# Kernel tuning notes

Measured on AMD Instinct MI355X. Metric: run time of the kernel, lower is better.

Reference implementation:

```python
import jax, jax.numpy as jnp
import numpy as np

N_NODES = 100000
N_EDGES = 640000
HIDDEN = 128


def setup_inputs() -> dict:
    key = jax.random.key(0)
    k1, k2, k3, k4 = jax.random.split(key, 4)
    node_emb = jax.random.normal(k1, (N_NODES, HIDDEN), dtype=jnp.float32)
    edge_index = jax.random.randint(k2, (2, N_EDGES), 0, N_NODES, dtype=jnp.int64)
    # edge head params: Linear(2H -> H), Linear(H -> 2)
    s1 = 1.0 / np.sqrt(2 * HIDDEN)
    s2 = 1.0 / np.sqrt(HIDDEN)
    W1 = jax.random.uniform(k3, (2 * HIDDEN, HIDDEN), jnp.float32, -s1, s1)
    b1 = jnp.zeros((HIDDEN,), jnp.float32)
    W2 = jax.random.uniform(k4, (HIDDEN, 2), jnp.float32, -s2, s2)
    b2 = jnp.zeros((2,), jnp.float32)
    return {"node_emb": node_emb, "edge_index": edge_index,
            "W1": W1, "b1": b1, "W2": W2, "b2": b2}


def reference(node_emb, edge_index, W1, b1, W2, b2):
    # gather src/dst node embeddings by edge_index (irregular gather)
    src, dst = edge_index[0], edge_index[1]
    edge_emb = jnp.concatenate([node_emb[src], node_emb[dst]], axis=-1)  # [E, 2H]
    # edge head: Linear -> ReLU -> (Dropout = identity in eval) -> Linear
    h = jax.nn.relu(edge_emb @ W1 + b1)  # [E, H]
    flow_pred = h @ W2 + b2              # [E, 2]
    return flow_pred
```

## Files before the change

kernel.cpp:

```cpp
#include <hip/hip_runtime.h>

typedef __attribute__((ext_vector_type(8))) short short8;
typedef __attribute__((ext_vector_type(4))) float floatx4;

static __device__ __forceinline__ unsigned short f2bf(float f) {
    union { float f; unsigned int u; } v; v.f = f;
    unsigned int u = v.u;
    return (unsigned short)((u + 0x7FFFu + ((u >> 16) & 1u)) >> 16);
}

__global__ void cvt_nodes_kernel(const float* __restrict__ x,
                                 unsigned short* __restrict__ y, int n4) {
    int i = blockIdx.x * blockDim.x + threadIdx.x;
    if (i >= n4) return;
    const float4 v = ((const float4*)x)[i];
    ushort4 o;
    o.x = f2bf(v.x); o.y = f2bf(v.y); o.z = f2bf(v.z); o.w = f2bf(v.w);
    ((ushort4*)y)[i] = o;
}

__global__ void cvt_w1t_kernel(const float* __restrict__ w1,
                               unsigned short* __restrict__ w1t) {
    int t = blockIdx.x * blockDim.x + threadIdx.x;
    int k = t >> 7;
    int n = t & 127;
    w1t[n * 256 + k] = f2bf(w1[t]);
}

#define LDSW 136

__global__ __launch_bounds__(256, 2) void edge_mlp_kernel(
    const unsigned short* __restrict__ nodes,
    const unsigned short* __restrict__ w1t,
    const int* __restrict__ eidx,
    const float* __restrict__ b1,
    const float* __restrict__ w2,
    const float* __restrict__ b2,
    float* __restrict__ out,
    int E, int n_nodes)
{
    __shared__ unsigned short sB[128 * LDSW];

    const int tid = threadIdx.x;
    const int lane = tid & 63;
    const int wave = tid >> 6;
    const int l15 = lane & 15;
    const int lq  = lane >> 4;
    const long e0 = (long)blockIdx.x * 256 + (long)wave * 64;

    int offs[4], offd[4];
#pragma unroll
    for (int rt = 0; rt < 4; rt++) {
        long e = e0 + rt * 16 + l15;
        if (e >= E) e = E - 1;
        int s = eidx[e];
        int d = eidx[(long)E + e];
        s = (s < 0) ? 0 : (s >= n_nodes ? n_nodes - 1 : s);
        d = (d < 0) ? 0 : (d >= n_nodes ? n_nodes - 1 : d);
        offs[rt] = s << 8;
        offd[rt] = d << 8;
    }
    const char* nbase = (const char*)nodes;
    const int lko = lq * 16;

    floatx4 acc[4][8];
#pragma unroll
    for (int rt = 0; rt < 4; rt++)
#pragma unroll
        for (int t = 0; t < 8; t++) acc[rt][t] = (floatx4){0.f, 0.f, 0.f, 0.f};

    short8 a_cur[4], a_nxt[4];
#pragma unroll
    for (int rt = 0; rt < 4; rt++)
        a_cur[rt] = *(const short8*)(nbase + offs[rt] + lko);

    for (int ch = 0; ch < 2; ch++) {
        if (ch) __syncthreads();
        for (int c = tid; c < 2048; c += 256) {
            int n = c >> 4, kk = (c & 15) << 3;
            *(short8*)(&sB[n * LDSW + kk]) =
                *(const short8*)(&w1t[n * 256 + ch * 128 + kk]);
        }
        __syncthreads();

#pragma unroll
        for (int k2 = 0; k2 < 4; k2++) {
            const int ks = ch * 4 + k2;
            if (ks < 7) {
                const int ksn = ks + 1;
                const int cb = ((ksn & 3) * 64) + lko;
#pragma unroll
                for (int rt = 0; rt < 4; rt++)
                    a_nxt[rt] = *(const short8*)(
                        nbase + ((ksn < 4) ? offs[rt] : offd[rt]) + cb);
            }
            const int bko = k2 * 32 + lq * 8;
#pragma unroll
            for (int t = 0; t < 8; t++) {
                short8 b = *(const short8*)(&sB[(t * 16 + l15) * LDSW + bko]);
#pragma unroll
                for (int rt = 0; rt < 4; rt++)
                    acc[rt][t] = __builtin_amdgcn_mfma_f32_16x16x32_bf16(
                        a_cur[rt], b, acc[rt][t], 0, 0, 0);
            }
#pragma unroll
            for (int rt = 0; rt < 4; rt++) a_cur[rt] = a_nxt[rt];
        }
    }

    float b1v[8], w20[8], w21[8];
#pragma unroll
    for (int t = 0; t < 8; t++) {
        int c = t * 16 + l15;
        b1v[t] = b1[c];
        w20[t] = w2[c * 2];
        w21[t] = w2[c * 2 + 1];
    }
    const float bias0 = b2[0], bias1 = b2[1];
#pragma unroll
    for (int rt = 0; rt < 4; rt++) {
#pragma unroll
        for (int i = 0; i < 4; i++) {
            float p0 = 0.f, p1 = 0.f;
#pragma unroll
            for (int t = 0; t < 8; t++) {
                float h = acc[rt][t][i] + b1v[t];
                h = fmaxf(h, 0.f);
                p0 = fmaf(h, w20[t], p0);
                p1 = fmaf(h, w21[t], p1);
            }
#pragma unroll
            for (int m = 1; m < 16; m <<= 1) {
                p0 += __shfl_xor(p0, m, 64);
                p1 += __shfl_xor(p1, m, 64);
            }
            if (l15 == 0) {
                long e = e0 + rt * 16 + lq * 4 + i;
                if (e < E) {
                    float2 o;
                    o.x = p0 + bias0;
                    o.y = p1 + bias1;
                    *(float2*)(&out[e * 2]) = o;
                }
            }
        }
    }
}

extern "C" void kernel_launch(void* const* d_in, const int* in_sizes, int n_in,
                              void* d_out, int out_size, void* d_ws, size_t ws_size,
                              hipStream_t stream) {
    const float* node_emb = (const float*)d_in[0];
    const int*   eidx     = (const int*)d_in[1];
    const float* W1       = (const float*)d_in[2];
    const float* b1       = (const float*)d_in[3];
    const float* W2       = (const float*)d_in[4];
    const float* b2       = (const float*)d_in[5];
    float* out = (float*)d_out;

    const int n_node_elems = in_sizes[0];
    const int n_nodes = n_node_elems / 128;
    const int E = in_sizes[1] / 2;

    unsigned short* nodes_bf16 = (unsigned short*)d_ws;
    unsigned short* w1t =
        (unsigned short*)((char*)d_ws + (size_t)n_node_elems * 2);

    const int n4 = n_node_elems / 4;
    cvt_nodes_kernel<<<(n4 + 255) / 256, 256, 0, stream>>>(node_emb, nodes_bf16, n4);
    cvt_w1t_kernel<<<128, 256, 0, stream>>>(W1, w1t);

    const int nblk = (E + 255) / 256;
    edge_mlp_kernel<<<nblk, 256, 0, stream>>>(nodes_bf16, w1t, eidx,
                                              b1, W2, b2, out, E, n_nodes);
}
```

Measured before the change: 188.8 us.

## Split output columns across wave pairs, swizzle LDS, merge conversion kernels

```diff
diff --git a/kernel.cpp b/kernel.cpp
--- a/kernel.cpp
+++ b/kernel.cpp
@@ -9,27 +9,38 @@
     return (unsigned short)((u + 0x7FFFu + ((u >> 16) & 1u)) >> 16);
 }
 
-__global__ void cvt_nodes_kernel(const float* __restrict__ x,
-                                 unsigned short* __restrict__ y, int n4) {
-    int i = blockIdx.x * blockDim.x + threadIdx.x;
-    if (i >= n4) return;
-    const float4 v = ((const float4*)x)[i];
-    ushort4 o;
-    o.x = f2bf(v.x); o.y = f2bf(v.y); o.z = f2bf(v.z); o.w = f2bf(v.w);
-    ((ushort4*)y)[i] = o;
+__global__ void cvt_kernel(const float* __restrict__ x, unsigned short* __restrict__ y,
+                           int n4, const float* __restrict__ w1,
+                           unsigned short* __restrict__ w1t, int nblk_nodes) {
+    __shared__ unsigned short sT[32 * 130];
+    if ((int)blockIdx.x < nblk_nodes) {
+        int i = blockIdx.x * 256 + threadIdx.x;
+        if (i >= n4) return;
+        const float4 v = ((const float4*)x)[i];
+        ushort4 o;
+        o.x = f2bf(v.x); o.y = f2bf(v.y); o.z = f2bf(v.z); o.w = f2bf(v.w);
+        ((ushort4*)y)[i] = o;
+    } else {
+        const int b = blockIdx.x - nblk_nodes;
+        const int k0 = b * 32;
+        const int tid = threadIdx.x;
+#pragma unroll
+        for (int i = 0; i < 16; i++) {
+            int idx = tid + i * 256;
+            int k = idx >> 7, n = idx & 127;
+            sT[k * 130 + n] = f2bf(w1[(k0 + k) * 128 + n]);
+        }
+        __syncthreads();
+#pragma unroll
+        for (int i = 0; i < 16; i++) {
+            int idx = tid + i * 256;
+            int n = idx >> 5, k = idx & 31;
+            w1t[n * 256 + k0 + k] = sT[k * 130 + n];
+        }
+    }
 }
 
-__global__ void cvt_w1t_kernel(const float* __restrict__ w1,
-                               unsigned short* __restrict__ w1t) {
-    int t = blockIdx.x * blockDim.x + threadIdx.x;
-    int k = t >> 7;
-    int n = t & 127;
-    w1t[n * 256 + k] = f2bf(w1[t]);
-}
-
-#define LDSW 136
-
-__global__ __launch_bounds__(256, 2) void edge_mlp_kernel(
+__global__ __launch_bounds__(512, 4) void edge_mlp_kernel(
     const unsigned short* __restrict__ nodes,
     const unsigned short* __restrict__ w1t,
     const int* __restrict__ eidx,
@@ -39,14 +50,17 @@
     float* __restrict__ out,
     int E, int n_nodes)
 {
-    __shared__ unsigned short sB[128 * LDSW];
+    __shared__ unsigned short sB[128 * 128];
+    __shared__ float2 sP[2][256];
 
-    const int tid = threadIdx.x;
+    const int tid  = threadIdx.x;
     const int lane = tid & 63;
     const int wave = tid >> 6;
-    const int l15 = lane & 15;
-    const int lq  = lane >> 4;
-    const long e0 = (long)blockIdx.x * 256 + (long)wave * 64;
+    const int g    = wave >> 1;
+    const int half = wave & 1;
+    const int l15  = lane & 15;
+    const int lq   = lane >> 4;
+    const long e0  = (long)blockIdx.x * 256 + g * 64;
 
     int offs[4], offd[4];
 #pragma unroll
@@ -61,25 +75,27 @@
         offd[rt] = d << 8;
     }
     const char* nbase = (const char*)nodes;
-    const int lko = lq * 16;
+    const int lbo = lq * 16;
 
-    floatx4 acc[4][8];
+    floatx4 acc[4][4];
 #pragma unroll
     for (int rt = 0; rt < 4; rt++)
 #pragma unroll
-        for (int t = 0; t < 8; t++) acc[rt][t] = (floatx4){0.f, 0.f, 0.f, 0.f};
+        for (int t = 0; t < 4; t++) acc[rt][t] = (floatx4){0.f, 0.f, 0.f, 0.f};
 
     short8 a_cur[4], a_nxt[4];
 #pragma unroll
     for (int rt = 0; rt < 4; rt++)
-        a_cur[rt] = *(const short8*)(nbase + offs[rt] + lko);
+        a_cur[rt] = *(const short8*)(nbase + offs[rt] + lbo);
 
     for (int ch = 0; ch < 2; ch++) {
         if (ch) __syncthreads();
-        for (int c = tid; c < 2048; c += 256) {
-            int n = c >> 4, kk = (c & 15) << 3;
-            *(short8*)(&sB[n * LDSW + kk]) =
-                *(const short8*)(&w1t[n * 256 + ch * 128 + kk]);
+#pragma unroll
+        for (int i = 0; i < 4; i++) {
+            int u = tid + i * 512;
+            int n = u >> 4, s = u & 15;
+            *(short8*)&sB[n * 128 + ((s ^ n) & 15) * 8] =
+                *(const short8*)&w1t[n * 256 + ch * 128 + s * 8];
         }
         __syncthreads();
 
@@ -88,16 +104,17 @@
             const int ks = ch * 4 + k2;
             if (ks < 7) {
                 const int ksn = ks + 1;
-                const int cb = ((ksn & 3) * 64) + lko;
+                const int cb = (ksn & 3) * 64 + lbo;
+                const int* of = (ksn < 4) ? offs : offd;
 #pragma unroll
                 for (int rt = 0; rt < 4; rt++)
-                    a_nxt[rt] = *(const short8*)(
-                        nbase + ((ksn < 4) ? offs[rt] : offd[rt]) + cb);
+                    a_nxt[rt] = *(const short8*)(nbase + of[rt] + cb);
             }
-            const int bko = k2 * 32 + lq * 8;
 #pragma unroll
-            for (int t = 0; t < 8; t++) {
-                short8 b = *(const short8*)(&sB[(t * 16 + l15) * LDSW + bko]);
+            for (int t = 0; t < 4; t++) {
+                const int n = (half * 4 + t) * 16 + l15;
+                const int sl = (k2 * 4 + lq) ^ l15;
+                short8 b = *(const short8*)&sB[n * 128 + sl * 8];
 #pragma unroll
                 for (int rt = 0; rt < 4; rt++)
                     acc[rt][t] = __builtin_amdgcn_mfma_f32_16x16x32_bf16(
@@ -108,22 +125,21 @@
         }
     }
 
-    float b1v[8], w20[8], w21[8];
+    float b1v[4], w20[4], w21[4];
 #pragma unroll
-    for (int t = 0; t < 8; t++) {
-        int c = t * 16 + l15;
+    for (int t = 0; t < 4; t++) {
+        int c = (half * 4 + t) * 16 + l15;
         b1v[t] = b1[c];
         w20[t] = w2[c * 2];
         w21[t] = w2[c * 2 + 1];
     }
-    const float bias0 = b2[0], bias1 = b2[1];
 #pragma unroll
     for (int rt = 0; rt < 4; rt++) {
 #pragma unroll
         for (int i = 0; i < 4; i++) {
             float p0 = 0.f, p1 = 0.f;
 #pragma unroll
-            for (int t = 0; t < 8; t++) {
+            for (int t = 0; t < 4; t++) {
                 float h = acc[rt][t][i] + b1v[t];
                 h = fmaxf(h, 0.f);
                 p0 = fmaf(h, w20[t], p0);
@@ -135,14 +151,20 @@
                 p1 += __shfl_xor(p1, m, 64);
             }
             if (l15 == 0) {
-                long e = e0 + rt * 16 + lq * 4 + i;
-                if (e < E) {
-                    float2 o;
-                    o.x = p0 + bias0;
-                    o.y = p1 + bias1;
-                    *(float2*)(&out[e * 2]) = o;
-                }
+                float2 o; o.x = p0; o.y = p1;
+                sP[half][g * 64 + rt * 16 + lq * 4 + i] = o;
             }
+        }
+    }
+    __syncthreads();
+
+    {
+        const int el = tid >> 1, chn = tid & 1;
+        const long e = (long)blockIdx.x * 256 + el;
+        if (e < E) {
+            const float* p0 = (const float*)&sP[0][el];
+            const float* p1 = (const float*)&sP[1][el];
+            out[e * 2 + chn] = p0[chn] + p1[chn] + b2[chn];
         }
     }
 }
@@ -167,10 +189,11 @@
         (unsigned short*)((char*)d_ws + (size_t)n_node_elems * 2);
 
     const int n4 = n_node_elems / 4;
-    cvt_nodes_kernel<<<(n4 + 255) / 256, 256, 0, stream>>>(node_emb, nodes_bf16, n4);
-    cvt_w1t_kernel<<<128, 256, 0, stream>>>(W1, w1t);
+    const int nblk_nodes = (n4 + 255) / 256;
+    cvt_kernel<<<nblk_nodes + 8, 256, 0, stream>>>(node_emb, nodes_bf16, n4,
+                                                   W1, w1t, nblk_nodes);
 
     const int nblk = (E + 255) / 256;
-    edge_mlp_kernel<<<nblk, 256, 0, stream>>>(nodes_bf16, w1t, eidx,
+    edge_mlp_kernel<<<nblk, 512, 0, stream>>>(nodes_bf16, w1t, eidx,
                                               b1, W2, b2, out, E, n_nodes);
 }
```

Measured after the change: 190.2 us. No clear change (+0.8%).
